# Optimization experiments

Hardware: AMD Instinct MI355X
Metric: run time of the kernel (lower is better)

Reference implementation:

```python
import jax, jax.numpy as jnp
import numpy as np
from jax import lax

PAIRS = ((0, 1), (1, 2), (2, 3), (3, 0))


def _apply_1q(state, U, w):
    # state: (N,2,2,2,2); wire w lives at axis w+1
    state = jnp.moveaxis(state, w + 1, -1)
    if U.ndim == 2:  # shared gate across batch
        state = jnp.einsum('ij,...j->...i', U, state)
    else:            # per-batch gate (encoder), U: (N,2,2)
        state = jnp.einsum('nij,n...j->n...i', U, state)
    return jnp.moveaxis(state, -1, w + 1)


def _ry_mat(theta):
    # torchquantum RY: [[cos(t/2), -sin(t/2)], [sin(t/2), cos(t/2)]]
    h = theta * 0.5
    c, s = jnp.cos(h), jnp.sin(h)
    return jnp.stack([jnp.stack([c, -s], -1), jnp.stack([s, c], -1)], -2).astype(jnp.complex64)


def _rz_mat(theta):
    # torchquantum RZ: diag(e^{-i t/2}, e^{+i t/2})
    h = (theta * 0.5).astype(jnp.complex64)
    e0, e1 = jnp.exp(-1j * h), jnp.exp(1j * h)
    z = jnp.zeros_like(e0)
    return jnp.stack([jnp.stack([e0, z], -1), jnp.stack([z, e1], -1)], -2)


def _cnot(state, c, t):
    st = jnp.moveaxis(state, (c + 1, t + 1), (-2, -1))
    st = jnp.stack([st[..., 0, :], st[..., 1, ::-1]], axis=-2)
    return jnp.moveaxis(st, (-2, -1), (c + 1, t + 1))


def _ansatz(state, p, a, b):
    state = _apply_1q(state, _ry_mat(p[0]), a)
    state = _apply_1q(state, _rz_mat(p[1]), a)
    state = _apply_1q(state, _ry_mat(p[2]), b)
    state = _apply_1q(state, _rz_mat(p[3]), b)
    state = _cnot(state, a, b)
    state = _apply_1q(state, _ry_mat(p[4]), a)
    state = _apply_1q(state, _rz_mat(p[5]), a)
    state = _apply_1q(state, _ry_mat(p[6]), b)
    return state


def _circuit(angles, qp):
    # angles: (N,4) in [0,pi]; qp: (2,7). Returns <Z_w> per wire: (N,4)
    N = angles.shape[0]
    state = jnp.zeros((N, 2, 2, 2, 2), jnp.complex64).at[:, 0, 0, 0, 0].set(1.0)
    for w in range(4):  # GeneralEncoder: RY(x_w) on wire w
        state = _apply_1q(state, _ry_mat(angles[:, w]), w)
    for layer in range(2):
        for (a, b) in PAIRS:
            state = _ansatz(state, qp[layer], a, b)
    probs = state.real ** 2 + state.imag ** 2
    exps = []
    for w in range(4):
        axes = tuple(ax for ax in range(1, 5) if ax != w + 1)
        m = probs.sum(axis=axes)  # (N,2)
        exps.append(m[:, 0] - m[:, 1])
    return jnp.stack(exps, axis=-1)


def _conv(x, w, b):
    y = lax.conv_general_dilated(x, w, (1, 1), 'SAME',
                                 dimension_numbers=('NCHW', 'OIHW', 'NCHW'))
    return y + b[None, :, None, None]


def _pool(x):
    return lax.reduce_window(x, -jnp.inf, lax.max, (1, 1, 2, 2), (1, 1, 2, 2), 'VALID')


def setup_inputs() -> dict:
    key = jax.random.key(0)
    ks = jax.random.split(key, 16)
    r = lambda k, sh, sc=0.1: (jax.random.normal(k, sh, dtype=jnp.float32) * sc)
    return {
        'x': jax.random.normal(ks[0], (2048, 1, 28, 28), dtype=jnp.float32),
        'conv1_w': r(ks[1], (64, 1, 3, 3)), 'conv1_b': r(ks[2], (64,)),
        'conv2_w': r(ks[3], (16, 64, 3, 3)), 'conv2_b': r(ks[4], (16,)),
        'conv3_w': r(ks[5], (4, 16, 3, 3)), 'conv3_b': r(ks[6], (4,)),
        'q_params': jax.random.uniform(ks[7], (2, 7), dtype=jnp.float32),
        'fc1_w': r(ks[8], (64, 196)), 'fc1_b': r(ks[9], (64,)),
        'fc2_w': r(ks[10], (128, 64)), 'fc2_b': r(ks[11], (128,)),
        'fc3_w': r(ks[12], (64, 128)), 'fc3_b': r(ks[13], (64,)),
        'fc4_w': r(ks[14], (10, 64)), 'fc4_b': r(ks[15], (10,)),
    }


def reference(x, conv1_w, conv1_b, conv2_w, conv2_b, conv3_w, conv3_b,
              q_params, fc1_w, fc1_b, fc2_w, fc2_b, fc3_w, fc3_b, fc4_w, fc4_b):
    h = _pool(jax.nn.relu(_conv(x, conv1_w, conv1_b)))       # (B,64,14,14)
    h = _pool(jax.nn.relu(_conv(h, conv2_w, conv2_b)))       # (B,16,7,7)
    h = jax.nn.leaky_relu(_conv(h, conv3_w, conv3_b), 0.01)  # (B,4,7,7)
    B, C, H, W = h.shape
    # 1x1 patches: (B, H*W, C) -> flatten over patches
    patches = h.reshape(B, C, H * W).transpose(0, 2, 1).reshape(B * H * W, C)
    angles = jax.nn.sigmoid(patches) * np.float32(np.pi)
    q = _circuit(angles, q_params)            # (B*49, 4)
    q = q.reshape(B, H * W * C)               # (B, 196)
    h = jax.nn.relu(q @ fc1_w.T + fc1_b)
    h = h @ fc2_w.T + fc2_b
    h = jax.nn.relu(h @ fc3_w.T + fc3_b)
    return h @ fc4_w.T + fc4_b
```

## Files before the change

kernel.cpp:

```cpp
#include <hip/hip_runtime.h>
#include <hip/hip_bf16.h>
#include <math.h>

#define DEV __device__ __forceinline__

typedef __attribute__((ext_vector_type(4))) float f32x4;
typedef __attribute__((ext_vector_type(8))) short bf16x8;

DEV unsigned short f2bf(float v) {
    __hip_bfloat16 h = __float2bfloat16(v);
    return *reinterpret_cast<unsigned short*>(&h);
}
DEV unsigned pk2(float a, float b) {
    union { __hip_bfloat162 b2; unsigned u; } cv;
    cv.b2 = __float22bfloat162_rn(float2{a, b});
    return cv.u;
}

__global__ void prep_kernel(const float* __restrict__ w1,
                            const float* __restrict__ w2,
                            const float* __restrict__ fc1w,
                            const float* __restrict__ fc2w,
                            const float* __restrict__ fc3w,
                            const float* __restrict__ fc4w,
                            unsigned short* __restrict__ w1b,
                            unsigned short* __restrict__ w2b,
                            float* __restrict__ fc1t,
                            float* __restrict__ fc2t,
                            float* __restrict__ fc3t,
                            float* __restrict__ fc4t)
{
    int t = blockIdx.x * blockDim.x + threadIdx.x;
    int NT = gridDim.x * blockDim.x;
    for (int i = t; i < 2048; i += NT) {
        int j = i & 7, oc = (i >> 3) & 63, fqq = i >> 9;
        int tap = fqq * 8 + j;
        w1b[i] = tap < 9 ? f2bf(w1[oc * 9 + tap]) : (unsigned short)0;
    }
    for (int i = t; i < 9216; i += NT) {
        int j = i & 7, oc = (i >> 3) & 15, fq = (i >> 7) & 3, f = i >> 9;
        int tap = f >> 1, kk = f & 1;
        int ic = kk * 32 + fq * 8 + j;
        w2b[i] = f2bf(w2[(oc * 64 + ic) * 9 + tap]);
    }
    for (int i = t; i < 12544; i += NT) { int j = i / 196, k = i % 196; fc1t[k * 64 + j] = fc1w[i]; }
    for (int i = t; i < 8192;  i += NT) { int j = i / 64,  k = i % 64;  fc2t[k * 128 + j] = fc2w[i]; }
    for (int i = t; i < 8192;  i += NT) { int j = i / 128, k = i % 128; fc3t[k * 64 + j] = fc3w[i]; }
    for (int i = t; i < 640;   i += NT) { int j = i / 64,  k = i % 64;  fc4t[k * 10 + j] = fc4w[i]; }
}

__global__ __launch_bounds__(256, 3) void conv12_kernel(
    const float* __restrict__ x,
    const float* __restrict__ b1, const unsigned short* __restrict__ w1b,
    const unsigned short* __restrict__ w2b,
    const float* __restrict__ b2, float* __restrict__ out2)
{
    __shared__ __align__(128) char lds_all[36864];
    float* pin = (float*)lds_all;
    char* in_b = lds_all + 4096;
    float* d_l = (float*)in_b;
    int t = threadIdx.x, lane = t & 63, wv = t >> 6;
    int fq = lane >> 4, fr = lane & 15;
    int n = blockIdx.x;

    bf16x8 bfrag[18];
    const bf16x8* wb = (const bf16x8*)w2b;
    #pragma unroll
    for (int f = 0; f < 18; ++f) bfrag[f] = wb[(f * 4 + fq) * 16 + fr];
    bf16x8 w1f[4];
    const bf16x8* wb1 = (const bf16x8*)w1b;
    float b1v[4];
    #pragma unroll
    for (int nt = 0; nt < 4; ++nt) {
        w1f[nt] = wb1[fq * 64 + nt * 16 + fr];
        b1v[nt] = b1[nt * 16 + fr];
    }

    for (int i = t; i < 2048; i += 256) ((f32x4*)in_b)[i] = f32x4{0.f, 0.f, 0.f, 0.f};
    for (int i = t; i < 1020; i += 256) pin[i] = 0.f;
    __syncthreads();
    for (int i = t; i < 784; i += 256) pin[(i / 28 + 1) * 34 + (i % 28) + 1] = x[n * 784 + i];
    __syncthreads();

    for (int tile = wv; tile < 49; tile += 4) {
        int pooledA = tile * 4 + (fr >> 2);
        int pyA = pooledA / 14, pxA = pooledA - pyA * 14;
        int Y = 2 * pyA + ((fr >> 1) & 1), X = 2 * pxA + (fr & 1);
        const float* ap = pin + Y * 34 + X + (fq == 1 ? 70 : 0);
        float q0 = ap[0],  q1 = ap[1],  q2 = ap[2];
        float q3 = ap[34], q4 = ap[35], q5 = ap[36];
        float q6 = ap[68], q7 = ap[69];
        union { uint4 u; bf16x8 v; } A;
        A.u.x = pk2(q0, q1); A.u.y = pk2(q2, q3);
        A.u.z = pk2(q4, q5); A.u.w = pk2(q6, q7);

        f32x4 a0 = {0.f,0.f,0.f,0.f}, a1 = {0.f,0.f,0.f,0.f},
              a2 = {0.f,0.f,0.f,0.f}, a3 = {0.f,0.f,0.f,0.f};
        a0 = __builtin_amdgcn_mfma_f32_16x16x32_bf16(A.v, w1f[0], a0, 0, 0, 0);
        a1 = __builtin_amdgcn_mfma_f32_16x16x32_bf16(A.v, w1f[1], a1, 0, 0, 0);
        a2 = __builtin_amdgcn_mfma_f32_16x16x32_bf16(A.v, w1f[2], a2, 0, 0, 0);
        a3 = __builtin_amdgcn_mfma_f32_16x16x32_bf16(A.v, w1f[3], a3, 0, 0, 0);

        int pooledD = tile * 4 + fq;
        int pyD = pooledD / 14, pxD = pooledD - pyD * 14;
        int grid = (pyD + 1) * 16 + (pxD + 1);
        unsigned swz = (unsigned)(grid & 7) << 4;
        unsigned base = (unsigned)grid * 128 + (unsigned)fr * 2;
        float v0 = fmaxf(fmaxf(fmaxf(a0[0], a0[1]), fmaxf(a0[2], a0[3])) + b1v[0], 0.f);
        float v1 = fmaxf(fmaxf(fmaxf(a1[0], a1[1]), fmaxf(a1[2], a1[3])) + b1v[1], 0.f);
        float v2 = fmaxf(fmaxf(fmaxf(a2[0], a2[1]), fmaxf(a2[2], a2[3])) + b1v[2], 0.f);
        float v3 = fmaxf(fmaxf(fmaxf(a3[0], a3[1]), fmaxf(a3[2], a3[3])) + b1v[3], 0.f);
        unsigned p01 = pk2(v0, v1), p23 = pk2(v2, v3);
        *(unsigned short*)(in_b + ((base +  0) ^ swz)) = (unsigned short)p01;
        *(unsigned short*)(in_b + ((base + 32) ^ swz)) = (unsigned short)(p01 >> 16);
        *(unsigned short*)(in_b + ((base + 64) ^ swz)) = (unsigned short)p23;
        *(unsigned short*)(in_b + ((base + 96) ^ swz)) = (unsigned short)(p23 >> 16);
    }
    __syncthreads();

    for (int r = 0; r < 4; ++r) {
        int tile = r * 4 + wv;
        bool tv = tile < 13;
        f32x4 acc = {0.f, 0.f, 0.f, 0.f};
        int pd0 = tile * 16 + fq * 4;
        if (tv) {
            int pos = tile * 16 + fr; pos = pos > 195 ? 195 : pos;
            int y = pos / 14, xx = pos - y * 14;
            int g0 = y * 16 + xx;
            int vb = g0 * 128 + fq * 16;
            #pragma unroll
            for (int ky = 0; ky < 3; ++ky)
                #pragma unroll
                for (int kx = 0; kx < 3; ++kx) {
                    int dg = ky * 16 + kx;
                    int msk = ((g0 + dg) & 7) << 4;
                    int lin = vb + dg * 128;
                    bf16x8 a0 = *(const bf16x8*)(in_b + (lin ^ msk));
                    acc = __builtin_amdgcn_mfma_f32_16x16x32_bf16(a0, bfrag[(ky * 3 + kx) * 2], acc, 0, 0, 0);
                    bf16x8 a1 = *(const bf16x8*)(in_b + ((lin | 64) ^ msk));
                    acc = __builtin_amdgcn_mfma_f32_16x16x32_bf16(a1, bfrag[(ky * 3 + kx) * 2 + 1], acc, 0, 0, 0);
                }
        }
        __syncthreads();
        if (tv) {
            #pragma unroll
            for (int reg = 0; reg < 4; ++reg) {
                int pd = pd0 + reg;
                if (pd < 196) d_l[pd * 17 + fr] = acc[reg];
            }
        }
        __syncthreads();
    }

    float* op = out2 + (size_t)n * 784;
    for (int i = t; i < 784; i += 256) {
        int oc = i & 15, p7 = i >> 4;
        int y7 = p7 / 7, x7 = p7 % 7;
        int p00 = (2 * y7) * 14 + 2 * x7;
        float m = fmaxf(fmaxf(d_l[p00 * 17 + oc], d_l[(p00 + 1) * 17 + oc]),
                        fmaxf(d_l[(p00 + 14) * 17 + oc], d_l[(p00 + 15) * 17 + oc]));
        op[oc * 49 + p7] = fmaxf(m + b2[oc], 0.f);
    }
}

template<int B>
DEV void ry_b(float* sr, float* si, float c, float s) {
    #pragma unroll
    for (int i = 0; i < 16; ++i) if (!(i & B)) {
        int j = i | B;
        float r0 = sr[i], m0 = si[i], r1 = sr[j], m1 = si[j];
        sr[i] = c * r0 - s * r1;  si[i] = c * m0 - s * m1;
        sr[j] = s * r0 + c * r1;  si[j] = s * m0 + c * m1;
    }
}
template<int B>
DEV void rz_b(float* sr, float* si, float c, float s) {
    #pragma unroll
    for (int i = 0; i < 16; ++i) {
        float xr = sr[i], xi = si[i];
        if (!(i & B)) { sr[i] = c * xr + s * xi;  si[i] = c * xi - s * xr; }
        else          { sr[i] = c * xr - s * xi;  si[i] = c * xi + s * xr; }
    }
}
template<int BC, int BT>
DEV void cnot_b(float* sr, float* si) {
    #pragma unroll
    for (int i = 0; i < 16; ++i) if ((i & BC) && !(i & BT)) {
        int j = i | BT;
        float tr = sr[i]; sr[i] = sr[j]; sr[j] = tr;
        float ti = si[i]; si[i] = si[j]; si[j] = ti;
    }
}
template<int A, int Bw>
DEV void ansatz(float* sr, float* si, const float* cc, const float* ss) {
    constexpr int BA = 8 >> A, BB = 8 >> Bw;
    ry_b<BA>(sr, si, cc[0], ss[0]);
    rz_b<BA>(sr, si, cc[1], ss[1]);
    ry_b<BB>(sr, si, cc[2], ss[2]);
    rz_b<BB>(sr, si, cc[3], ss[3]);
    cnot_b<BA, BB>(sr, si);
    ry_b<BA>(sr, si, cc[4], ss[4]);
    rz_b<BA>(sr, si, cc[5], ss[5]);
    ry_b<BB>(sr, si, cc[6], ss[6]);
}

__global__ __launch_bounds__(256) void qconv_kernel(
    const float* __restrict__ out2, const float* __restrict__ w3,
    const float* __restrict__ b3, const float* __restrict__ qp,
    float* __restrict__ q)
{
    int gid = blockIdx.x * 256 + threadIdx.x;
    int n = gid / 49, pp = gid % 49;
    int py = pp / 7, px = pp % 7;
    const float* in = out2 + n * 784;

    float acc[4] = { b3[0], b3[1], b3[2], b3[3] };
    for (int ic = 0; ic < 16; ++ic) {
        #pragma unroll
        for (int ky = 0; ky < 3; ++ky) {
            int yy = py + ky - 1;
            int yc = min(max(yy, 0), 6);
            #pragma unroll
            for (int kx = 0; kx < 3; ++kx) {
                int xx = px + kx - 1;
                int xc = min(max(xx, 0), 6);
                bool valid = ((unsigned)yy < 7u) && ((unsigned)xx < 7u);
                float v = in[ic * 49 + yc * 7 + xc];
                v = valid ? v : 0.f;
                #pragma unroll
                for (int c = 0; c < 4; ++c)
                    acc[c] = fmaf(w3[(c * 16 + ic) * 9 + ky * 3 + kx], v, acc[c]);
            }
        }
    }
    float h[4];
    #pragma unroll
    for (int c = 0; c < 4; ++c) {
        float z = acc[c];
        z = z > 0.f ? z : 0.01f * z;
        float sg = 1.f / (1.f + __expf(-z));
        h[c] = 1.5707963267948966f * sg;
    }

    float sr[16], si[16];
    #pragma unroll
    for (int i = 0; i < 16; ++i) { sr[i] = 0.f; si[i] = 0.f; }
    sr[0] = 1.f;

    float ce, se;
    __sincosf(h[0], &se, &ce); ry_b<8>(sr, si, ce, se);
    __sincosf(h[1], &se, &ce); ry_b<4>(sr, si, ce, se);
    __sincosf(h[2], &se, &ce); ry_b<2>(sr, si, ce, se);
    __sincosf(h[3], &se, &ce); ry_b<1>(sr, si, ce, se);

    float cs0[7], sn0[7], cs1[7], sn1[7];
    #pragma unroll
    for (int k = 0; k < 7; ++k) {
        __sincosf(qp[k] * 0.5f, &sn0[k], &cs0[k]);
        __sincosf(qp[7 + k] * 0.5f, &sn1[k], &cs1[k]);
    }
    ansatz<0, 1>(sr, si, cs0, sn0);
    ansatz<1, 2>(sr, si, cs0, sn0);
    ansatz<2, 3>(sr, si, cs0, sn0);
    ansatz<3, 0>(sr, si, cs0, sn0);
    ansatz<0, 1>(sr, si, cs1, sn1);
    ansatz<1, 2>(sr, si, cs1, sn1);
    ansatz<2, 3>(sr, si, cs1, sn1);
    ansatz<3, 0>(sr, si, cs1, sn1);

    float p[16];
    #pragma unroll
    for (int i = 0; i < 16; ++i) p[i] = sr[i] * sr[i] + si[i] * si[i];

    float* qo = q + n * 196 + pp * 4;
    #pragma unroll
    for (int w = 0; w < 4; ++w) {
        int B = 8 >> w;
        float e = 0.f;
        #pragma unroll
        for (int i = 0; i < 16; ++i) e += (i & B) ? -p[i] : p[i];
        qo[w] = e;
    }
}

__global__ __launch_bounds__(64) void fc_kernel(
    const float* __restrict__ q,
    const float* __restrict__ fc1t, const float* __restrict__ fb1,
    const float* __restrict__ fc2t, const float* __restrict__ fb2,
    const float* __restrict__ fc3t, const float* __restrict__ fb3,
    const float* __restrict__ fc4t, const float* __restrict__ fb4,
    float* __restrict__ out)
{
    __shared__ float qr[196], h1[64], h2[128], h3[64];
    int n = blockIdx.x, t = threadIdx.x;
    for (int i = t; i < 196; i += 64) qr[i] = q[n * 196 + i];
    __syncthreads();
    float a = fb1[t];
    for (int k = 0; k < 196; ++k) a = fmaf(fc1t[k * 64 + t], qr[k], a);
    h1[t] = fmaxf(a, 0.f);
    __syncthreads();
    float a0 = fb2[t], a1 = fb2[t + 64];
    for (int k = 0; k < 64; ++k) {
        float v = h1[k];
        a0 = fmaf(fc2t[k * 128 + t], v, a0);
        a1 = fmaf(fc2t[k * 128 + t + 64], v, a1);
    }
    h2[t] = a0; h2[t + 64] = a1;
    __syncthreads();
    a = fb3[t];
    for (int k = 0; k < 128; ++k) a = fmaf(fc3t[k * 64 + t], h2[k], a);
    h3[t] = fmaxf(a, 0.f);
    __syncthreads();
    if (t < 10) {
        a = fb4[t];
        for (int k = 0; k < 64; ++k) a = fmaf(fc4t[k * 10 + t], h3[k], a);
        out[n * 10 + t] = a;
    }
}

extern "C" void kernel_launch(void* const* d_in, const int* in_sizes, int n_in,
                              void* d_out, int out_size, void* d_ws, size_t ws_size,
                              hipStream_t stream) {
    const float* x      = (const float*)d_in[0];
    const float* c1w    = (const float*)d_in[1];
    const float* c1b    = (const float*)d_in[2];
    const float* c2w    = (const float*)d_in[3];
    const float* c2b    = (const float*)d_in[4];
    const float* c3w    = (const float*)d_in[5];
    const float* c3b    = (const float*)d_in[6];
    const float* qp     = (const float*)d_in[7];
    const float* fc1w   = (const float*)d_in[8];
    const float* fc1b   = (const float*)d_in[9];
    const float* fc2w   = (const float*)d_in[10];
    const float* fc2b   = (const float*)d_in[11];
    const float* fc3w   = (const float*)d_in[12];
    const float* fc3b   = (const float*)d_in[13];
    const float* fc4w   = (const float*)d_in[14];
    const float* fc4b   = (const float*)d_in[15];
    float* out = (float*)d_out;

    float* ws = (float*)d_ws;
    unsigned short* w2b = (unsigned short*)ws;
    unsigned short* w1b = (unsigned short*)(ws + 4608);
    float* fc1t = ws + 5632;
    float* fc2t = fc1t + 12544;
    float* fc3t = fc2t + 8192;
    float* fc4t = fc3t + 8192;
    float* out2 = fc4t + 640;
    float* qbuf = out2 + (size_t)2048 * 784;

    prep_kernel<<<40, 256, 0, stream>>>(c1w, c2w, fc1w, fc2w, fc3w, fc4w,
                                        w1b, w2b, fc1t, fc2t, fc3t, fc4t);
    conv12_kernel<<<2048, 256, 0, stream>>>(x, c1b, w1b, w2b, c2b, out2);
    qconv_kernel<<<392, 256, 0, stream>>>(out2, c3w, c3b, qp, qbuf);
    fc_kernel<<<2048, 64, 0, stream>>>(qbuf, fc1t, fc1b, fc2t, fc2b,
                                       fc3t, fc3b, fc4t, fc4b, out);
}
```

Measured before the change: 70.95 us.

## Fuse conv2 pooling into MFMA epilogue and store padded channel-last output

Conv1 results are packed into one 8-byte LDS store per lane, with conv2 input channels permuted in the weight prep to match. Conv2 M-tiles are reordered so each group of four rows is one 2x2 pooling window, letting max-pool, bias and ReLU happen in registers. This removes the LDS staging pass and its barriers. Output is written as a zero-padded 9x9x16 channel-last buffer, so qconv reads float4 channel vectors without bounds checks, at the cost of a larger intermediate buffer and border zeroing.

Result: slower. 95.45 us (+34.5%).

```diff
diff --git a/kernel.cpp b/kernel.cpp
--- a/kernel.cpp
+++ b/kernel.cpp
@@ -40,7 +40,8 @@
     for (int i = t; i < 9216; i += NT) {
         int j = i & 7, oc = (i >> 3) & 15, fq = (i >> 7) & 3, f = i >> 9;
         int tap = f >> 1, kk = f & 1;
-        int ic = kk * 32 + fq * 8 + j;
+        int s = kk * 32 + fq * 8 + j;
+        int ic = (s & 3) * 16 + (s >> 2);
         w2b[i] = f2bf(w2[(oc * 64 + ic) * 9 + tap]);
     }
     for (int i = t; i < 12544; i += NT) { int j = i / 196, k = i % 196; fc1t[k * 64 + j] = fc1w[i]; }
@@ -58,7 +59,6 @@
     __shared__ __align__(128) char lds_all[36864];
     float* pin = (float*)lds_all;
     char* in_b = lds_all + 4096;
-    float* d_l = (float*)in_b;
     int t = threadIdx.x, lane = t & 63, wv = t >> 6;
     int fq = lane >> 4, fr = lane & 15;
     int n = blockIdx.x;
@@ -75,9 +75,20 @@
         w1f[nt] = wb1[fq * 64 + nt * 16 + fr];
         b1v[nt] = b1[nt * 16 + fr];
     }
+    float b2v = b2[fr];
 
     for (int i = t; i < 2048; i += 256) ((f32x4*)in_b)[i] = f32x4{0.f, 0.f, 0.f, 0.f};
     for (int i = t; i < 1020; i += 256) pin[i] = 0.f;
+    if (t < 128) {
+        int cell = t >> 2, comp = t & 3;
+        int pos;
+        if (cell < 9)       pos = cell;
+        else if (cell < 18) pos = 72 + (cell - 9);
+        else if (cell < 25) pos = (cell - 17) * 9;
+        else                pos = (cell - 24) * 9 + 8;
+        *reinterpret_cast<float4*>(out2 + (size_t)n * 1296 + pos * 16 + comp * 4)
+            = float4{0.f, 0.f, 0.f, 0.f};
+    }
     __syncthreads();
     for (int i = t; i < 784; i += 256) pin[(i / 28 + 1) * 34 + (i % 28) + 1] = x[n * 784 + i];
     __syncthreads();
@@ -101,65 +112,46 @@
         a2 = __builtin_amdgcn_mfma_f32_16x16x32_bf16(A.v, w1f[2], a2, 0, 0, 0);
         a3 = __builtin_amdgcn_mfma_f32_16x16x32_bf16(A.v, w1f[3], a3, 0, 0, 0);
 
-        int pooledD = tile * 4 + fq;
-        int pyD = pooledD / 14, pxD = pooledD - pyD * 14;
-        int grid = (pyD + 1) * 16 + (pxD + 1);
+        int pooled = tile * 4 + fq;
+        int py = pooled / 14, px = pooled - py * 14;
+        int grid = (py + 1) * 16 + (px + 1);
         unsigned swz = (unsigned)(grid & 7) << 4;
-        unsigned base = (unsigned)grid * 128 + (unsigned)fr * 2;
         float v0 = fmaxf(fmaxf(fmaxf(a0[0], a0[1]), fmaxf(a0[2], a0[3])) + b1v[0], 0.f);
         float v1 = fmaxf(fmaxf(fmaxf(a1[0], a1[1]), fmaxf(a1[2], a1[3])) + b1v[1], 0.f);
         float v2 = fmaxf(fmaxf(fmaxf(a2[0], a2[1]), fmaxf(a2[2], a2[3])) + b1v[2], 0.f);
         float v3 = fmaxf(fmaxf(fmaxf(a3[0], a3[1]), fmaxf(a3[2], a3[3])) + b1v[3], 0.f);
-        unsigned p01 = pk2(v0, v1), p23 = pk2(v2, v3);
-        *(unsigned short*)(in_b + ((base +  0) ^ swz)) = (unsigned short)p01;
-        *(unsigned short*)(in_b + ((base + 32) ^ swz)) = (unsigned short)(p01 >> 16);
-        *(unsigned short*)(in_b + ((base + 64) ^ swz)) = (unsigned short)p23;
-        *(unsigned short*)(in_b + ((base + 96) ^ swz)) = (unsigned short)(p23 >> 16);
-    }
-    __syncthreads();
-
-    for (int r = 0; r < 4; ++r) {
-        int tile = r * 4 + wv;
-        bool tv = tile < 13;
+        uint2 w; w.x = pk2(v0, v1); w.y = pk2(v2, v3);
+        *reinterpret_cast<uint2*>(in_b + (((unsigned)grid * 128 + (unsigned)fr * 8) ^ swz)) = w;
+    }
+    __syncthreads();
+
+    for (int tile = wv; tile < 13; tile += 4) {
         f32x4 acc = {0.f, 0.f, 0.f, 0.f};
-        int pd0 = tile * 16 + fq * 4;
-        if (tv) {
-            int pos = tile * 16 + fr; pos = pos > 195 ? 195 : pos;
-            int y = pos / 14, xx = pos - y * 14;
-            int g0 = y * 16 + xx;
-            int vb = g0 * 128 + fq * 16;
+        int pv = tile * 4 + (fr >> 2); pv = pv > 48 ? 48 : pv;
+        int sub = fr & 3;
+        int y7 = pv / 7, x7 = pv - y7 * 7;
+        int y = 2 * y7 + (sub >> 1), xx = 2 * x7 + (sub & 1);
+        int g0 = y * 16 + xx;
+        int vb = g0 * 128 + fq * 16;
+        #pragma unroll
+        for (int ky = 0; ky < 3; ++ky)
             #pragma unroll
-            for (int ky = 0; ky < 3; ++ky)
-                #pragma unroll
-                for (int kx = 0; kx < 3; ++kx) {
-                    int dg = ky * 16 + kx;
-                    int msk = ((g0 + dg) & 7) << 4;
-                    int lin = vb + dg * 128;
-                    bf16x8 a0 = *(const bf16x8*)(in_b + (lin ^ msk));
-                    acc = __builtin_amdgcn_mfma_f32_16x16x32_bf16(a0, bfrag[(ky * 3 + kx) * 2], acc, 0, 0, 0);
-                    bf16x8 a1 = *(const bf16x8*)(in_b + ((lin | 64) ^ msk));
-                    acc = __builtin_amdgcn_mfma_f32_16x16x32_bf16(a1, bfrag[(ky * 3 + kx) * 2 + 1], acc, 0, 0, 0);
-                }
+            for (int kx = 0; kx < 3; ++kx) {
+                int dg = ky * 16 + kx;
+                int msk = ((g0 + dg) & 7) << 4;
+                int lin = vb + dg * 128;
+                bf16x8 a0 = *(const bf16x8*)(in_b + (lin ^ msk));
+                acc = __builtin_amdgcn_mfma_f32_16x16x32_bf16(a0, bfrag[(ky * 3 + kx) * 2], acc, 0, 0, 0);
+                bf16x8 a1 = *(const bf16x8*)(in_b + ((lin | 64) ^ msk));
+                acc = __builtin_amdgcn_mfma_f32_16x16x32_bf16(a1, bfrag[(ky * 3 + kx) * 2 + 1], acc, 0, 0, 0);
+            }
+        int pooled2 = tile * 4 + fq;
+        if (pooled2 < 49) {
+            float m = fmaxf(fmaxf(acc[0], acc[1]), fmaxf(acc[2], acc[3]));
+            int y9 = pooled2 / 7, x9 = pooled2 - y9 * 7;
+            out2[(size_t)n * 1296 + ((y9 + 1) * 9 + (x9 + 1)) * 16 + fr] =
+                fmaxf(m + b2v, 0.f);
         }
-        __syncthreads();
-        if (tv) {
-            #pragma unroll
-            for (int reg = 0; reg < 4; ++reg) {
-                int pd = pd0 + reg;
-                if (pd < 196) d_l[pd * 17 + fr] = acc[reg];
-            }
-        }
-        __syncthreads();
-    }
-
-    float* op = out2 + (size_t)n * 784;
-    for (int i = t; i < 784; i += 256) {
-        int oc = i & 15, p7 = i >> 4;
-        int y7 = p7 / 7, x7 = p7 % 7;
-        int p00 = (2 * y7) * 14 + 2 * x7;
-        float m = fmaxf(fmaxf(d_l[p00 * 17 + oc], d_l[(p00 + 1) * 17 + oc]),
-                        fmaxf(d_l[(p00 + 14) * 17 + oc], d_l[(p00 + 15) * 17 + oc]));
-        op[oc * 49 + p7] = fmaxf(m + b2[oc], 0.f);
     }
 }
 
@@ -212,27 +204,27 @@
     int gid = blockIdx.x * 256 + threadIdx.x;
     int n = gid / 49, pp = gid % 49;
     int py = pp / 7, px = pp % 7;
-    const float* in = out2 + n * 784;
+    const float* in = out2 + (size_t)n * 1296;
 
     float acc[4] = { b3[0], b3[1], b3[2], b3[3] };
-    for (int ic = 0; ic < 16; ++ic) {
+    #pragma unroll
+    for (int ky = 0; ky < 3; ++ky)
         #pragma unroll
-        for (int ky = 0; ky < 3; ++ky) {
-            int yy = py + ky - 1;
-            int yc = min(max(yy, 0), 6);
+        for (int kx = 0; kx < 3; ++kx) {
+            const float* cp = in + ((py + ky) * 9 + (px + kx)) * 16;
             #pragma unroll
-            for (int kx = 0; kx < 3; ++kx) {
-                int xx = px + kx - 1;
-                int xc = min(max(xx, 0), 6);
-                bool valid = ((unsigned)yy < 7u) && ((unsigned)xx < 7u);
-                float v = in[ic * 49 + yc * 7 + xc];
-                v = valid ? v : 0.f;
+            for (int icq = 0; icq < 4; ++icq) {
+                float4 v = *reinterpret_cast<const float4*>(cp + icq * 4);
                 #pragma unroll
-                for (int c = 0; c < 4; ++c)
-                    acc[c] = fmaf(w3[(c * 16 + ic) * 9 + ky * 3 + kx], v, acc[c]);
+                for (int c = 0; c < 4; ++c) {
+                    const float* wc = w3 + (c * 16 + icq * 4) * 9 + ky * 3 + kx;
+                    acc[c] = fmaf(wc[0],  v.x, acc[c]);
+                    acc[c] = fmaf(wc[9],  v.y, acc[c]);
+                    acc[c] = fmaf(wc[18], v.z, acc[c]);
+                    acc[c] = fmaf(wc[27], v.w, acc[c]);
+                }
             }
         }
-    }
     float h[4];
     #pragma unroll
     for (int c = 0; c < 4; ++c) {
@@ -347,7 +339,7 @@
     float* fc3t = fc2t + 8192;
     float* fc4t = fc3t + 8192;
     float* out2 = fc4t + 640;
-    float* qbuf = out2 + (size_t)2048 * 784;
+    float* qbuf = out2 + (size_t)2048 * 1296;
 
     prep_kernel<<<40, 256, 0, stream>>>(c1w, c2w, fc1w, fc2w, fc3w, fc4w,
                                         w1b, w2b, fc1t, fc2t, fc3t, fc4t);
```
